# Optimization experiments

Hardware: AMD Instinct MI355X
Metric: run time of the kernel (lower is better)

The kernel has to match this reference:

```python
import jax, jax.numpy as jnp
import numpy as np

K = 1024          # num_embeddings
D = 64            # embedding_dim
COMMIT = 0.25
DIVERSITY = 0.1


def setup_inputs() -> dict:
    key = jax.random.key(0)
    k1, k2 = jax.random.split(key)
    inputs = jax.random.normal(k1, (64, D, 32, 32), dtype=jnp.float32)
    emb = jax.random.uniform(k2, (K, D), dtype=jnp.float32,
                             minval=-1.0 / K, maxval=1.0 / K)
    return {"inputs": inputs, "emb": emb}


def reference(inputs, emb):
    # NCHW -> NHWC, flatten to [N, D]
    x = jnp.transpose(inputs, (0, 2, 3, 1))          # [B,H,W,D]
    flat = x.reshape(-1, D)                           # [N,D]

    dist = (jnp.sum(flat * flat, axis=1, keepdims=True)
            + jnp.sum(emb * emb, axis=1)
            - 2.0 * flat @ emb.T)
    idx = jnp.argmin(dist, axis=1)                    # [N]
    encodings = jax.nn.one_hot(idx, K, dtype=flat.dtype)  # [N,K]

    # codebook lookup (equivalent to encodings @ emb)
    quantized = jnp.take(emb, idx, axis=0).reshape(x.shape)  # [B,H,W,D]

    sg = jax.lax.stop_gradient
    e_latent_loss = jnp.mean((sg(quantized) - x) ** 2)
    q_latent_loss = jnp.mean((quantized - sg(x)) ** 2)

    avg_probs = jnp.mean(encodings, axis=0)           # [K]
    perplexity = jnp.exp(-jnp.sum(avg_probs * jnp.log(avg_probs + 1e-10)))
    diversity_loss = DIVERSITY * (K - perplexity) / K

    loss = q_latent_loss + COMMIT * e_latent_loss + diversity_loss

    # straight-through estimator
    quantized_st = x + sg(quantized - x)
    quant_out = jnp.transpose(quantized_st, (0, 3, 1, 2))  # NHWC -> NCHW

    return loss, quant_out, perplexity, encodings, idx[:, None]
```

## Files before the change

### kernel.cpp

```cpp
#include <hip/hip_runtime.h>
#include <math.h>

typedef _Float16 half8 __attribute__((ext_vector_type(8)));
typedef float floatx4 __attribute__((ext_vector_type(4)));

namespace {
constexpr int Kc = 1024;
constexpr int Dd = 64;
constexpr float MARGIN = 4e-4f;

__device__ inline float np_sumsq64_s(const float* __restrict__ a, int st) {
#pragma clang fp contract(off)
    float r[8];
    #pragma unroll
    for (int j = 0; j < 8; ++j) r[j] = a[j * st] * a[j * st];
    #pragma unroll
    for (int i = 8; i < 64; i += 8) {
        #pragma unroll
        for (int j = 0; j < 8; ++j) {
            float s = a[(i + j) * st] * a[(i + j) * st];
            r[j] = r[j] + s;
        }
    }
    return ((r[0] + r[1]) + (r[2] + r[3])) + ((r[4] + r[5]) + (r[6] + r[7]));
}

__device__ inline float np_dist(const float* __restrict__ x, int xs,
                                const float* __restrict__ emb, int k,
                                float xx, float eek) {
    const float* e = emb + (size_t)k * Dd;
    float g = 0.f;
    #pragma unroll
    for (int d = 0; d < Dd; ++d) g = fmaf(x[d * xs], e[d], g);
    float A = xx + eek;
    return fmaf(-2.f, g, A);
}

__global__ void k_prep(const float* __restrict__ emb, float* __restrict__ ee,
                       _Float16* __restrict__ emb16) {
    int k = blockIdx.x * blockDim.x + threadIdx.x;
    const float* e = emb + (size_t)k * Dd;
    ee[k] = np_sumsq64_s(e, 1);
    #pragma unroll
    for (int d = 0; d < Dd; ++d) emb16[k * Dd + d] = (_Float16)e[d];
}

__global__ __launch_bounds__(256, 4) void k_main(
    const float* __restrict__ inputs, const float* __restrict__ emb,
    const float* __restrict__ ee_g, const _Float16* __restrict__ emb16,
    float* __restrict__ quant, float* __restrict__ enc, float* __restrict__ idx_out,
    unsigned int* __restrict__ hist, float* __restrict__ partials)
{
    __shared__ short  smemB[128 * 72];
    __shared__ float  eeS[Kc];
    __shared__ float  cDT[16][65], cD2T[16][65];
    __shared__ int    cIT[16][65], cI2T[16][65];
    __shared__ float  red[64];
    __shared__ int    bidxS[64];
    __shared__ int    flagged[64];
    __shared__ int    nflag;
    __shared__ float  fbD[256];
    __shared__ int    fbI[256];

    const int tid = threadIdx.x;
    const int w   = tid >> 6;
    const int ln  = tid & 63;
    const int lm  = ln & 15;
    const int lq  = ln >> 4;

    if (tid == 0) nflag = 0;
    #pragma unroll
    for (int i = 0; i < 4; ++i) eeS[tid + i * 256] = ee_g[tid + i * 256];

    const int nA = blockIdx.x * 64 + w * 16 + lm;
    const float* xA = inputs + (size_t)(nA >> 10) * (Dd * 1024) + (nA & 1023);
    half8 a0, a1;
    #pragma unroll
    for (int j = 0; j < 8; ++j) {
        a0[j] = (_Float16)xA[(lq * 8 + j) * 1024];
        a1[j] = (_Float16)xA[(lq * 8 + j + 32) * 1024];
    }

    float4* enc4 = (float4*)enc + (size_t)blockIdx.x * 16384 + tid;

    float b1[4], b2[4];
    int   i1[4], i2[4];
    #pragma unroll
    for (int r = 0; r < 4; ++r) { b1[r] = INFINITY; b2[r] = INFINITY; i1[r] = 0; i2[r] = 0; }

    for (int c = 0; c < 8; ++c) {
        __syncthreads();
        #pragma unroll
        for (int u = 0; u < 4; ++u) {
            int unit = u * 256 + tid;
            int row = unit >> 3, c8 = unit & 7;
            half8 v = *(const half8*)(emb16 + ((size_t)(c * 128 + row) * 64) + c8 * 8);
            *(half8*)(smemB + row * 72 + c8 * 8) = v;
        }
        __syncthreads();

        #pragma unroll
        for (int tt = 0; tt < 8; ++tt) {
            const int r = tt * 16 + lm;
            const int kn = c * 128 + r;
            const half8 bb0 = *(const half8*)(smemB + r * 72 + lq * 8);
            const half8 bb1 = *(const half8*)(smemB + r * 72 + 32 + lq * 8);
            floatx4 acc = {0.f, 0.f, 0.f, 0.f};
            acc = __builtin_amdgcn_mfma_f32_16x16x32_f16(a0, bb0, acc, 0, 0, 0);
            acc = __builtin_amdgcn_mfma_f32_16x16x32_f16(a1, bb1, acc, 0, 0, 0);
            const float eev = eeS[kn];
            #pragma unroll
            for (int r4i = 0; r4i < 4; ++r4i) {
                float s = fmaf(-2.f, acc[r4i], eev);
                bool lt1 = s < b1[r4i], lt2 = s < b2[r4i];
                b2[r4i] = lt1 ? b1[r4i] : (lt2 ? s : b2[r4i]);
                i2[r4i] = lt1 ? i1[r4i] : (lt2 ? kn : i2[r4i]);
                b1[r4i] = lt1 ? s : b1[r4i];
                i1[r4i] = lt1 ? kn : i1[r4i];
            }
            *enc4 = float4{0.f, 0.f, 0.f, 0.f};
            enc4 += 256;
        }
    }

    #pragma unroll
    for (int r = 0; r < 4; ++r) {
        int p = w * 16 + lq * 4 + r;
        cDT[lm][p] = b1[r]; cIT[lm][p] = i1[r];
        cD2T[lm][p] = b2[r]; cI2T[lm][p] = i2[r];
    }
    __syncthreads();

    if (tid < 64) {
        const int p = tid;
        const int n = blockIdx.x * 64 + p;
        const float* x = inputs + (size_t)(n >> 10) * (Dd * 1024) + (n & 1023);
        float amin = INFINITY;
        #pragma unroll
        for (int cc = 0; cc < 16; ++cc) amin = fminf(amin, cDT[cc][p]);
        const float M = amin + MARGIN;
        bool flag = false;
        #pragma unroll
        for (int cc = 0; cc < 16; ++cc) flag |= (cD2T[cc][p] <= M);
        if (flag) {
            int s = atomicAdd(&nflag, 1);
            flagged[s] = p;
        } else {
            const float xx = np_sumsq64_s(x, 1024);
            float bd = INFINITY; int bi = 0x7fffffff;
            for (int cc = 0; cc < 16; ++cc)
                if (cDT[cc][p] <= M) {
                    int k = cIT[cc][p];
                    float d = np_dist(x, 1024, emb, k, xx, eeS[k]);
                    if (d < bd || (d == bd && k < bi)) { bd = d; bi = k; }
                }
            bidxS[p] = bi;
            red[p] = bd;
            idx_out[n] = (float)bi;
            atomicAdd(hist + bi, 1u);
            enc[(size_t)n * Kc + bi] = 1.0f;
        }
    }
    __syncthreads();

    const int nf = nflag;
    for (int f = 0; f < nf; ++f) {
        const int p = flagged[f];
        const int n = blockIdx.x * 64 + p;
        const float* x = inputs + (size_t)(n >> 10) * (Dd * 1024) + (n & 1023);
        const float xx = np_sumsq64_s(x, 1024);
        float bd = INFINITY; int bi = 0;
        #pragma unroll
        for (int q = 0; q < 4; ++q) {
            int k = tid * 4 + q;
            float d = np_dist(x, 1024, emb, k, xx, eeS[k]);
            bool lt = d < bd;
            bd = lt ? d : bd; bi = lt ? k : bi;
        }
        fbD[tid] = bd; fbI[tid] = bi;
        __syncthreads();
        if (tid == 0) {
            float gd = INFINITY; int gi = 0;
            for (int t2 = 0; t2 < 256; ++t2)
                if (fbD[t2] < gd) { gd = fbD[t2]; gi = fbI[t2]; }
            bidxS[p] = gi;
            red[p] = gd;
            idx_out[n] = (float)gi;
            atomicAdd(hist + gi, 1u);
            enc[(size_t)n * Kc + gi] = 1.0f;
        }
        __syncthreads();
    }

    {
        const int n = blockIdx.x * 64 + ln;
        const int bi = bidxS[ln];
        float* qout = quant + (size_t)(n >> 10) * (Dd * 1024) + (n & 1023);
        const float4* eb = (const float4*)(emb + (size_t)bi * Dd);
        #pragma unroll
        for (int i = 0; i < 4; ++i) {
            float4 v = eb[w * 4 + i];
            const int d0 = w * 16 + i * 4;
            qout[(d0 + 0) * 1024] = v.x;
            qout[(d0 + 1) * 1024] = v.y;
            qout[(d0 + 2) * 1024] = v.z;
            qout[(d0 + 3) * 1024] = v.w;
        }
    }

    if (tid < 64) {
        float v = red[tid];
        #pragma unroll
        for (int off = 32; off > 0; off >>= 1) v += __shfl_down(v, off, 64);
        if (ln == 0) partials[blockIdx.x] = v;
    }
}

__global__ __launch_bounds__(1024) void k_fin(
    const unsigned int* __restrict__ hist, const float* __restrict__ partials,
    float* __restrict__ loss_out, float* __restrict__ perp_out)
{
    __shared__ double sd[1024];
    int tid = threadIdx.x;
    double p = (double)hist[tid] * (1.0 / 65536.0);
    sd[tid] = p * log(p + 1e-10);
    __syncthreads();
    for (int s = 512; s > 0; s >>= 1) {
        if (tid < s) sd[tid] += sd[tid + s];
        __syncthreads();
    }
    double ent = sd[0];
    __syncthreads();
    sd[tid] = (double)partials[tid];
    __syncthreads();
    for (int s = 512; s > 0; s >>= 1) {
        if (tid < s) sd[tid] += sd[tid + s];
        __syncthreads();
    }
    if (tid == 0) {
        double perp = exp(-ent);
        double mean = sd[0] * (1.0 / 4194304.0);
        double loss = 1.25 * mean + 0.1 * (1024.0 - perp) / 1024.0;
        loss_out[0] = (float)loss;
        perp_out[0] = (float)perp;
    }
}
}

extern "C" void kernel_launch(void* const* d_in, const int* in_sizes, int n_in,
                              void* d_out, int out_size, void* d_ws, size_t ws_size,
                              hipStream_t stream)
{
    const float* inputs = (const float*)d_in[0];
    const float* emb    = (const float*)d_in[1];
    float* out = (float*)d_out;

    float* loss_out = out;
    float* quant    = out + 1;
    float* perp_out = out + 1 + 4194304;
    float* enc      = out + 2 + 4194304;
    float* idx_out  = out + 2 + 4194304 + 67108864;

    unsigned int* hist = (unsigned int*)d_ws;
    float* partials    = (float*)d_ws + 1024;
    float* ee          = (float*)d_ws + 2048;
    _Float16* emb16    = (_Float16*)((float*)d_ws + 3072);

    hipMemsetAsync(d_ws, 0, 2048 * sizeof(float), stream);
    k_prep<<<Kc / 256, 256, 0, stream>>>(emb, ee, emb16);
    k_main<<<65536 / 64, 256, 0, stream>>>(inputs, emb, ee, emb16,
                                           quant, enc, idx_out, hist, partials);
    k_fin<<<1, 1024, 0, stream>>>(hist, partials, loss_out, perp_out);
}
```

Before: 459.2 us.

## Write one-hot rows in one nontemporal pass and cache inputs in LDS

The encodings output (256 MB) was zeroed inside the MFMA loop and then patched with a scattered 1.0 write. It is now written once at the end of the kernel, with the one-hot value placed in-register, using nontemporal float4 stores. The input vectors are kept in shared memory so the exact-distance refinement reads LDS instead of strided global memory. The second-best index tracking and the occupancy hint in launch_bounds are also dropped, which shifts register pressure and may change occupancy.

```diff
diff --git a/kernel.cpp b/kernel.cpp
--- a/kernel.cpp
+++ b/kernel.cpp
@@ -9,29 +9,35 @@
 constexpr int Dd = 64;
 constexpr float MARGIN = 4e-4f;
 
-__device__ inline float np_sumsq64_s(const float* __restrict__ a, int st) {
+__device__ inline float np_sumsq64(const float* __restrict__ a) {
 #pragma clang fp contract(off)
     float r[8];
     #pragma unroll
-    for (int j = 0; j < 8; ++j) r[j] = a[j * st] * a[j * st];
+    for (int j = 0; j < 8; ++j) r[j] = a[j] * a[j];
     #pragma unroll
     for (int i = 8; i < 64; i += 8) {
         #pragma unroll
         for (int j = 0; j < 8; ++j) {
-            float s = a[(i + j) * st] * a[(i + j) * st];
+            float s = a[i + j] * a[i + j];
             r[j] = r[j] + s;
         }
     }
     return ((r[0] + r[1]) + (r[2] + r[3])) + ((r[4] + r[5]) + (r[6] + r[7]));
 }
 
-__device__ inline float np_dist(const float* __restrict__ x, int xs,
+__device__ inline float np_dist(const float* __restrict__ x,
                                 const float* __restrict__ emb, int k,
                                 float xx, float eek) {
-    const float* e = emb + (size_t)k * Dd;
+    const float4* e4 = (const float4*)(emb + (size_t)k * Dd);
     float g = 0.f;
     #pragma unroll
-    for (int d = 0; d < Dd; ++d) g = fmaf(x[d * xs], e[d], g);
+    for (int i = 0; i < 16; ++i) {
+        float4 v = e4[i];
+        g = fmaf(x[i * 4 + 0], v.x, g);
+        g = fmaf(x[i * 4 + 1], v.y, g);
+        g = fmaf(x[i * 4 + 2], v.z, g);
+        g = fmaf(x[i * 4 + 3], v.w, g);
+    }
     float A = xx + eek;
     return fmaf(-2.f, g, A);
 }
@@ -40,12 +46,12 @@
                        _Float16* __restrict__ emb16) {
     int k = blockIdx.x * blockDim.x + threadIdx.x;
     const float* e = emb + (size_t)k * Dd;
-    ee[k] = np_sumsq64_s(e, 1);
+    ee[k] = np_sumsq64(e);
     #pragma unroll
     for (int d = 0; d < Dd; ++d) emb16[k * Dd + d] = (_Float16)e[d];
 }
 
-__global__ __launch_bounds__(256, 4) void k_main(
+__global__ __launch_bounds__(256) void k_main(
     const float* __restrict__ inputs, const float* __restrict__ emb,
     const float* __restrict__ ee_g, const _Float16* __restrict__ emb16,
     float* __restrict__ quant, float* __restrict__ enc, float* __restrict__ idx_out,
@@ -53,8 +59,9 @@
 {
     __shared__ short  smemB[128 * 72];
     __shared__ float  eeS[Kc];
+    __shared__ float  xS[64][65];
     __shared__ float  cDT[16][65], cD2T[16][65];
-    __shared__ int    cIT[16][65], cI2T[16][65];
+    __shared__ int    cIT[16][65];
     __shared__ float  red[64];
     __shared__ int    bidxS[64];
     __shared__ int    flagged[64];
@@ -72,21 +79,24 @@
     #pragma unroll
     for (int i = 0; i < 4; ++i) eeS[tid + i * 256] = ee_g[tid + i * 256];
 
-    const int nA = blockIdx.x * 64 + w * 16 + lm;
+    const int pA = w * 16 + lm;
+    const int nA = blockIdx.x * 64 + pA;
     const float* xA = inputs + (size_t)(nA >> 10) * (Dd * 1024) + (nA & 1023);
     half8 a0, a1;
     #pragma unroll
     for (int j = 0; j < 8; ++j) {
-        a0[j] = (_Float16)xA[(lq * 8 + j) * 1024];
-        a1[j] = (_Float16)xA[(lq * 8 + j + 32) * 1024];
-    }
-
-    float4* enc4 = (float4*)enc + (size_t)blockIdx.x * 16384 + tid;
+        float v0 = xA[(lq * 8 + j) * 1024];
+        float v1 = xA[(lq * 8 + j + 32) * 1024];
+        a0[j] = (_Float16)v0;
+        a1[j] = (_Float16)v1;
+        xS[pA][lq * 8 + j]      = v0;
+        xS[pA][lq * 8 + j + 32] = v1;
+    }
 
     float b1[4], b2[4];
-    int   i1[4], i2[4];
-    #pragma unroll
-    for (int r = 0; r < 4; ++r) { b1[r] = INFINITY; b2[r] = INFINITY; i1[r] = 0; i2[r] = 0; }
+    int   i1[4];
+    #pragma unroll
+    for (int r = 0; r < 4; ++r) { b1[r] = INFINITY; b2[r] = INFINITY; i1[r] = 0; }
 
     for (int c = 0; c < 8; ++c) {
         __syncthreads();
@@ -110,31 +120,27 @@
             acc = __builtin_amdgcn_mfma_f32_16x16x32_f16(a1, bb1, acc, 0, 0, 0);
             const float eev = eeS[kn];
             #pragma unroll
-            for (int r4i = 0; r4i < 4; ++r4i) {
-                float s = fmaf(-2.f, acc[r4i], eev);
-                bool lt1 = s < b1[r4i], lt2 = s < b2[r4i];
-                b2[r4i] = lt1 ? b1[r4i] : (lt2 ? s : b2[r4i]);
-                i2[r4i] = lt1 ? i1[r4i] : (lt2 ? kn : i2[r4i]);
-                b1[r4i] = lt1 ? s : b1[r4i];
-                i1[r4i] = lt1 ? kn : i1[r4i];
+            for (int r4 = 0; r4 < 4; ++r4) {
+                float s = fmaf(-2.f, acc[r4], eev);
+                bool lt1 = s < b1[r4], lt2 = s < b2[r4];
+                b2[r4] = lt1 ? b1[r4] : (lt2 ? s : b2[r4]);
+                b1[r4] = lt1 ? s : b1[r4];
+                i1[r4] = lt1 ? kn : i1[r4];
             }
-            *enc4 = float4{0.f, 0.f, 0.f, 0.f};
-            enc4 += 256;
-        }
-    }
+        }
+    }
+    __syncthreads();
 
     #pragma unroll
     for (int r = 0; r < 4; ++r) {
         int p = w * 16 + lq * 4 + r;
-        cDT[lm][p] = b1[r]; cIT[lm][p] = i1[r];
-        cD2T[lm][p] = b2[r]; cI2T[lm][p] = i2[r];
+        cDT[lm][p] = b1[r]; cIT[lm][p] = i1[r]; cD2T[lm][p] = b2[r];
     }
     __syncthreads();
 
     if (tid < 64) {
         const int p = tid;
         const int n = blockIdx.x * 64 + p;
-        const float* x = inputs + (size_t)(n >> 10) * (Dd * 1024) + (n & 1023);
         float amin = INFINITY;
         #pragma unroll
         for (int cc = 0; cc < 16; ++cc) amin = fminf(amin, cDT[cc][p]);
@@ -146,19 +152,18 @@
             int s = atomicAdd(&nflag, 1);
             flagged[s] = p;
         } else {
-            const float xx = np_sumsq64_s(x, 1024);
+            const float xx = np_sumsq64(&xS[p][0]);
             float bd = INFINITY; int bi = 0x7fffffff;
             for (int cc = 0; cc < 16; ++cc)
                 if (cDT[cc][p] <= M) {
                     int k = cIT[cc][p];
-                    float d = np_dist(x, 1024, emb, k, xx, eeS[k]);
+                    float d = np_dist(&xS[p][0], emb, k, xx, eeS[k]);
                     if (d < bd || (d == bd && k < bi)) { bd = d; bi = k; }
                 }
             bidxS[p] = bi;
             red[p] = bd;
             idx_out[n] = (float)bi;
             atomicAdd(hist + bi, 1u);
-            enc[(size_t)n * Kc + bi] = 1.0f;
         }
     }
     __syncthreads();
@@ -166,14 +171,13 @@
     const int nf = nflag;
     for (int f = 0; f < nf; ++f) {
         const int p = flagged[f];
-        const int n = blockIdx.x * 64 + p;
-        const float* x = inputs + (size_t)(n >> 10) * (Dd * 1024) + (n & 1023);
-        const float xx = np_sumsq64_s(x, 1024);
+        const float* xp = &xS[p][0];
+        const float xx = np_sumsq64(xp);
         float bd = INFINITY; int bi = 0;
         #pragma unroll
         for (int q = 0; q < 4; ++q) {
             int k = tid * 4 + q;
-            float d = np_dist(x, 1024, emb, k, xx, eeS[k]);
+            float d = np_dist(xp, emb, k, xx, eeS[k]);
             bool lt = d < bd;
             bd = lt ? d : bd; bi = lt ? k : bi;
         }
@@ -185,11 +189,17 @@
                 if (fbD[t2] < gd) { gd = fbD[t2]; gi = fbI[t2]; }
             bidxS[p] = gi;
             red[p] = gd;
-            idx_out[n] = (float)gi;
+            idx_out[blockIdx.x * 64 + p] = (float)gi;
             atomicAdd(hist + gi, 1u);
-            enc[(size_t)n * Kc + gi] = 1.0f;
-        }
-        __syncthreads();
+        }
+        __syncthreads();
+    }
+
+    if (tid < 64) {
+        float v = red[tid];
+        #pragma unroll
+        for (int off = 32; off > 0; off >>= 1) v += __shfl_down(v, off, 64);
+        if (ln == 0) partials[blockIdx.x] = v;
     }
 
     {
@@ -208,11 +218,18 @@
         }
     }
 
-    if (tid < 64) {
-        float v = red[tid];
-        #pragma unroll
-        for (int off = 32; off > 0; off >>= 1) v += __shfl_down(v, off, 64);
-        if (ln == 0) partials[blockIdx.x] = v;
+    {
+        const int p = tid >> 2, q = tid & 3;
+        const int bi = bidxS[p];
+        const int ft = bi >> 2;
+        const int it = ft >> 2, qt = ft & 3, et = bi & 3;
+        floatx4* erow = (floatx4*)enc + ((size_t)(blockIdx.x * 64 + p)) * 256;
+        #pragma unroll 8
+        for (int i = 0; i < 64; ++i) {
+            floatx4 v = {0.f, 0.f, 0.f, 0.f};
+            if (q == qt && i == it) v[et] = 1.0f;
+            __builtin_nontemporal_store(v, &erow[i * 4 + q]);
+        }
     }
 }
 
@@ -266,7 +283,7 @@
     float* ee          = (float*)d_ws + 2048;
     _Float16* emb16    = (_Float16*)((float*)d_ws + 3072);
 
-    hipMemsetAsync(d_ws, 0, 2048 * sizeof(float), stream);
+    (void)hipMemsetAsync(d_ws, 0, 2048 * sizeof(float), stream);
     k_prep<<<Kc / 256, 256, 0, stream>>>(emb, ee, emb16);
     k_main<<<65536 / 64, 256, 0, stream>>>(inputs, emb, ee, emb16,
                                            quant, enc, idx_out, hist, partials);
```

New measurement: 477.3 us. 1.04x slower.

## Move one-hot encoding writes into a separate streaming kernel

Applied to the files above, without the earlier changes.

Removes the interleaved zero-fill of the 256MB one-hot encodings buffer from the distance/argmin kernel and writes it in a dedicated kernel that reads the indices and emits each row with the one set directly. This avoids the double write (zero then scattered 1.0) and decouples the store-bound phase from the MFMA phase. It also drops the unused second-best index tracking and the occupancy hint from launch bounds. The extra launch rereads indices and serializes the store-bound pass after compute instead of overlapping it.

```diff
diff --git a/kernel.cpp b/kernel.cpp
--- a/kernel.cpp
+++ b/kernel.cpp
@@ -30,7 +30,7 @@
                                 float xx, float eek) {
     const float* e = emb + (size_t)k * Dd;
     float g = 0.f;
-    #pragma unroll
+    #pragma unroll 8
     for (int d = 0; d < Dd; ++d) g = fmaf(x[d * xs], e[d], g);
     float A = xx + eek;
     return fmaf(-2.f, g, A);
@@ -45,16 +45,16 @@
     for (int d = 0; d < Dd; ++d) emb16[k * Dd + d] = (_Float16)e[d];
 }
 
-__global__ __launch_bounds__(256, 4) void k_main(
+__global__ __launch_bounds__(256) void k_main(
     const float* __restrict__ inputs, const float* __restrict__ emb,
     const float* __restrict__ ee_g, const _Float16* __restrict__ emb16,
-    float* __restrict__ quant, float* __restrict__ enc, float* __restrict__ idx_out,
+    float* __restrict__ quant, float* __restrict__ idx_out,
     unsigned int* __restrict__ hist, float* __restrict__ partials)
 {
     __shared__ short  smemB[128 * 72];
     __shared__ float  eeS[Kc];
     __shared__ float  cDT[16][65], cD2T[16][65];
-    __shared__ int    cIT[16][65], cI2T[16][65];
+    __shared__ int    cIT[16][65];
     __shared__ float  red[64];
     __shared__ int    bidxS[64];
     __shared__ int    flagged[64];
@@ -81,12 +81,10 @@
         a1[j] = (_Float16)xA[(lq * 8 + j + 32) * 1024];
     }
 
-    float4* enc4 = (float4*)enc + (size_t)blockIdx.x * 16384 + tid;
-
     float b1[4], b2[4];
-    int   i1[4], i2[4];
-    #pragma unroll
-    for (int r = 0; r < 4; ++r) { b1[r] = INFINITY; b2[r] = INFINITY; i1[r] = 0; i2[r] = 0; }
+    int   i1[4];
+    #pragma unroll
+    for (int r = 0; r < 4; ++r) { b1[r] = INFINITY; b2[r] = INFINITY; i1[r] = 0; }
 
     for (int c = 0; c < 8; ++c) {
         __syncthreads();
@@ -110,24 +108,21 @@
             acc = __builtin_amdgcn_mfma_f32_16x16x32_f16(a1, bb1, acc, 0, 0, 0);
             const float eev = eeS[kn];
             #pragma unroll
-            for (int r4i = 0; r4i < 4; ++r4i) {
-                float s = fmaf(-2.f, acc[r4i], eev);
-                bool lt1 = s < b1[r4i], lt2 = s < b2[r4i];
-                b2[r4i] = lt1 ? b1[r4i] : (lt2 ? s : b2[r4i]);
-                i2[r4i] = lt1 ? i1[r4i] : (lt2 ? kn : i2[r4i]);
-                b1[r4i] = lt1 ? s : b1[r4i];
-                i1[r4i] = lt1 ? kn : i1[r4i];
+            for (int r4 = 0; r4 < 4; ++r4) {
+                float s = fmaf(-2.f, acc[r4], eev);
+                bool lt1 = s < b1[r4], lt2 = s < b2[r4];
+                b2[r4] = lt1 ? b1[r4] : (lt2 ? s : b2[r4]);
+                b1[r4] = lt1 ? s : b1[r4];
+                i1[r4] = lt1 ? kn : i1[r4];
             }
-            *enc4 = float4{0.f, 0.f, 0.f, 0.f};
-            enc4 += 256;
-        }
-    }
+        }
+    }
+    __syncthreads();
 
     #pragma unroll
     for (int r = 0; r < 4; ++r) {
         int p = w * 16 + lq * 4 + r;
-        cDT[lm][p] = b1[r]; cIT[lm][p] = i1[r];
-        cD2T[lm][p] = b2[r]; cI2T[lm][p] = i2[r];
+        cDT[lm][p] = b1[r]; cIT[lm][p] = i1[r]; cD2T[lm][p] = b2[r];
     }
     __syncthreads();
 
@@ -158,7 +153,6 @@
             red[p] = bd;
             idx_out[n] = (float)bi;
             atomicAdd(hist + bi, 1u);
-            enc[(size_t)n * Kc + bi] = 1.0f;
         }
     }
     __syncthreads();
@@ -187,9 +181,15 @@
             red[p] = gd;
             idx_out[n] = (float)gi;
             atomicAdd(hist + gi, 1u);
-            enc[(size_t)n * Kc + gi] = 1.0f;
-        }
-        __syncthreads();
+        }
+        __syncthreads();
+    }
+
+    if (tid < 64) {
+        float v = red[tid];
+        #pragma unroll
+        for (int off = 32; off > 0; off >>= 1) v += __shfl_down(v, off, 64);
+        if (ln == 0) partials[blockIdx.x] = v;
     }
 
     {
@@ -207,12 +207,27 @@
             qout[(d0 + 3) * 1024] = v.w;
         }
     }
-
-    if (tid < 64) {
-        float v = red[tid];
-        #pragma unroll
-        for (int off = 32; off > 0; off >>= 1) v += __shfl_down(v, off, 64);
-        if (ln == 0) partials[blockIdx.x] = v;
+}
+
+__global__ __launch_bounds__(256) void k_enc(
+    const float* __restrict__ idx_out, float* __restrict__ enc)
+{
+    __shared__ int idxS[32];
+    const int tid = threadIdx.x;
+    const int base = blockIdx.x * 32;
+    if (tid < 32) idxS[tid] = (int)idx_out[base + tid];
+    __syncthreads();
+
+    const int p = tid >> 3, q = tid & 7;
+    const int bi = idxS[p];
+    const int ft = bi >> 2;
+    const int it = ft >> 3, qt = ft & 7, et = bi & 3;
+    floatx4* erow = (floatx4*)enc + ((size_t)(base + p)) * 256;
+    #pragma unroll 8
+    for (int i = 0; i < 32; ++i) {
+        floatx4 v = {0.f, 0.f, 0.f, 0.f};
+        if (q == qt && i == it) v[et] = 1.0f;
+        erow[i * 8 + q] = v;
     }
 }
 
@@ -266,9 +281,10 @@
     float* ee          = (float*)d_ws + 2048;
     _Float16* emb16    = (_Float16*)((float*)d_ws + 3072);
 
-    hipMemsetAsync(d_ws, 0, 2048 * sizeof(float), stream);
+    (void)hipMemsetAsync(d_ws, 0, 2048 * sizeof(float), stream);
     k_prep<<<Kc / 256, 256, 0, stream>>>(emb, ee, emb16);
     k_main<<<65536 / 64, 256, 0, stream>>>(inputs, emb, ee, emb16,
-                                           quant, enc, idx_out, hist, partials);
+                                           quant, idx_out, hist, partials);
+    k_enc<<<65536 / 32, 256, 0, stream>>>(idx_out, enc);
     k_fin<<<1, 1024, 0, stream>>>(hist, partials, loss_out, perp_out);
 }
```

New measurement: 498.2 us. 1.08x slower.
